# Kernel tuning notes

Measured on AMD Instinct MI355X. Metric: run time of the kernel, lower is better.

## Reference

```python
import jax, jax.numpy as jnp
import numpy as np

B, S, E, H = 2, 2048, 1024, 16
D = E // H  # head dim = 64
NEG_INF = -1e30


def alibi_slopes(n_head):
    # standard ALiBi slopes: 2^(-8*i/n_head), i = 1..n_head
    return jnp.asarray([2.0 ** (-8.0 * (i + 1) / n_head) for i in range(n_head)], dtype=jnp.float32)


def setup_inputs() -> dict:
    key = jax.random.key(0)
    ks = jax.random.split(key, 5)
    scale = 0.02
    return {
        "x": jax.random.normal(ks[0], (B, S, E), dtype=jnp.float32),
        "W_kqv": jax.random.normal(ks[1], (E, 3 * E), dtype=jnp.float32) * scale,
        "b_kqv": jnp.zeros((3 * E,), dtype=jnp.float32),
        "W_proj": jax.random.normal(ks[2], (E, E), dtype=jnp.float32) * scale,
        "b_proj": jnp.zeros((E,), dtype=jnp.float32),
        "slopes": alibi_slopes(H),
    }


def reference(x, W_kqv, b_kqv, W_proj, b_proj, slopes):
    b, s, e = x.shape
    kqv = x @ W_kqv + b_kqv                       # [b, s, 3e]
    k, q, v = jnp.split(kqv, 3, axis=-1)          # split order: k, q, v
    k = k.reshape(b, s, H, D)
    q = q.reshape(b, s, H, D)
    v = v.reshape(b, s, H, D)
    attn = jnp.einsum("bqhd,bkhd->bhqk", q, k) * (1.0 / jnp.sqrt(jnp.float32(D)))
    # ALiBi bias: slope_h * (j - i) for j <= i, -inf above diagonal (causal)
    i = jnp.arange(s)[:, None]
    j = jnp.arange(s)[None, :]
    rel = (j - i).astype(jnp.float32)             # [s, s]
    bias = slopes[:, None, None] * jnp.tril(rel)  # [h, s, s]
    bias = jnp.where(j > i, NEG_INF, bias)
    attn = jax.nn.softmax(attn + bias[None], axis=-1)
    # dropout is identity in eval mode
    y = jnp.einsum("bhqk,bkhd->bqhd", attn, v).reshape(b, s, e)
    return y @ W_proj + b_proj
```

## Files before the change

### kernel.cpp

```cpp
#include <hip/hip_runtime.h>

typedef unsigned short u16;
typedef float f32x4 __attribute__((ext_vector_type(4)));
typedef __bf16 bfx8 __attribute__((ext_vector_type(8)));
typedef __bf16 bfx4 __attribute__((ext_vector_type(4)));
typedef u16 u16x8 __attribute__((ext_vector_type(8)));
typedef u16 u16x4 __attribute__((ext_vector_type(4)));

#define B_ 2
#define S_ 2048
#define E_ 1024
#define H_ 16
#define D_ 64

__device__ __forceinline__ u16 f2bf(float f) {
  unsigned u = __float_as_uint(f);
  u = u + 0x7FFFu + ((u >> 16) & 1u);
  return (u16)(u >> 16);
}

__device__ __forceinline__ int swz128(int o) { return o ^ ((o >> 3) & 0x70); }

__device__ __forceinline__ void gload16(const void* g, void* l) {
  __builtin_amdgcn_global_load_lds((const __attribute__((address_space(1))) void*)g,
                                   (__attribute__((address_space(3))) void*)l, 16, 0, 0);
}

__global__ __launch_bounds__(256) void prep(const float* __restrict__ x,
                                            const float* __restrict__ Wk,
                                            const float* __restrict__ Wp, u16* __restrict__ xb,
                                            u16* __restrict__ wkt, u16* __restrict__ wpt) {
  __shared__ float tile[64][65];
  const int id = blockIdx.x, tid = threadIdx.x;
  if (id < 2048) {
    const float4* in4 = reinterpret_cast<const float4*>(x);
    u16x4* out4 = reinterpret_cast<u16x4*>(xb);
    int i = id * 256 + tid;
#pragma unroll
    for (int p = 0; p < 2; ++p, i += 524288) {
      const float4 v = in4[i];
      u16x4 o = {f2bf(v.x), f2bf(v.y), f2bf(v.z), f2bf(v.w)};
      out4[i] = o;
    }
    return;
  }
  const float* in;
  u16* out;
  int R, C, bx, by;
  if (id < 2816) {
    const int t = id - 2048;
    in = Wk; out = wkt; R = 1024; C = 3072; bx = t % 48; by = t / 48;
  } else {
    const int t = id - 2816;
    in = Wp; out = wpt; R = 1024; C = 1024; bx = t & 15; by = t >> 4;
  }
  const int ct = bx * 64, rt = by * 64;
#pragma unroll
  for (int p = 0; p < 4; ++p) {
    int f = p * 256 + tid;
    int row = f >> 4, c4 = (f & 15) << 2;
    const float4 v = *reinterpret_cast<const float4*>(in + (size_t)(rt + row) * C + ct + c4);
    tile[row][c4 + 0] = v.x; tile[row][c4 + 1] = v.y;
    tile[row][c4 + 2] = v.z; tile[row][c4 + 3] = v.w;
  }
  __syncthreads();
#pragma unroll
  for (int p = 0; p < 4; ++p) {
    int g = p * 256 + tid;
    int orow = g >> 4, k4 = (g & 15) << 2;
    u16x4 o = {f2bf(tile[k4 + 0][orow]), f2bf(tile[k4 + 1][orow]),
               f2bf(tile[k4 + 2][orow]), f2bf(tile[k4 + 3][orow])};
    *reinterpret_cast<u16x4*>(out + (size_t)(ct + orow) * R + rt + k4) = o;
  }
}

__global__ __launch_bounds__(256) void gemm_kqv(const u16* __restrict__ A,
                                                const u16* __restrict__ Bt,
                                                const float* __restrict__ bias, int M, int N, int K,
                                                u16* __restrict__ outK, u16* __restrict__ outQ,
                                                u16* __restrict__ outVt) {
  __shared__ __align__(16) u16 sA[128 * 64];
  __shared__ __align__(16) u16 sB[128 * 64];
  const int tid = threadIdx.x, lane = tid & 63;
  const int wave = tid >> 6, wr = wave >> 1, wc = wave & 1;
  int lin = blockIdx.y * gridDim.x + blockIdx.x;
  const int nwg = gridDim.x * gridDim.y;
  if ((nwg & 7) == 0) {
    const int cpx = nwg >> 3;
    lin = (lin & 7) * cpx + (lin >> 3);
  }
  const int bm = (lin / gridDim.x) * 128, bn = (lin % gridDim.x) * 128;
  const int r8 = lane >> 3, c16 = (lane & 7) ^ r8;
  f32x4 acc[4][4] = {};
  for (int k0 = 0; k0 < K; k0 += 64) {
#pragma unroll
    for (int i = 0; i < 4; ++i) {
      const int c = wave * 4 + i;
      const int row = c * 8 + r8;
      gload16(A + (size_t)(bm + row) * K + k0 + c16 * 8, (char*)sA + c * 1024);
      gload16(Bt + (size_t)(bn + row) * K + k0 + c16 * 8, (char*)sB + c * 1024);
    }
    __syncthreads();
#pragma unroll
    for (int kc = 0; kc < 2; ++kc) {
      bfx8 af[4], bf[4];
#pragma unroll
      for (int mf = 0; mf < 4; ++mf) {
        int o = swz128(((wr * 64 + mf * 16 + (lane & 15)) << 7) + kc * 64 + ((lane >> 4) << 4));
        af[mf] = *reinterpret_cast<const bfx8*>(reinterpret_cast<const char*>(sA) + o);
      }
#pragma unroll
      for (int nf = 0; nf < 4; ++nf) {
        int o = swz128(((wc * 64 + nf * 16 + (lane & 15)) << 7) + kc * 64 + ((lane >> 4) << 4));
        bf[nf] = *reinterpret_cast<const bfx8*>(reinterpret_cast<const char*>(sB) + o);
      }
#pragma unroll
      for (int mf = 0; mf < 4; ++mf)
#pragma unroll
        for (int nf = 0; nf < 4; ++nf)
          acc[mf][nf] = __builtin_amdgcn_mfma_f32_16x16x32_bf16(af[mf], bf[nf], acc[mf][nf], 0, 0, 0);
    }
    __syncthreads();
  }
#pragma unroll
  for (int mf = 0; mf < 4; ++mf)
#pragma unroll
    for (int nf = 0; nf < 4; ++nf)
#pragma unroll
      for (int r = 0; r < 4; ++r) {
        const int row = bm + wr * 64 + mf * 16 + ((lane >> 4) << 2) + r;
        const int col = bn + wc * 64 + nf * 16 + (lane & 15);
        const float v = acc[mf][nf][r] + bias[col];
        const int chunk = col >> 10, w = col & 1023, h = w >> 6, dd = w & 63;
        const int b = row >> 11, s = row & 2047;
        const int bh = b * H_ + h;
        if (chunk == 0)
          outK[((size_t)bh * S_ + s) * D_ + dd] = f2bf(v);
        else if (chunk == 1)
          outQ[((size_t)bh * S_ + s) * D_ + dd] = f2bf(v);
        else
          outVt[((size_t)bh * D_ + dd) * S_ + s] = f2bf(v);
      }
}

__global__ __launch_bounds__(512) void gemm_proj(const u16* __restrict__ A,
                                                 const u16* __restrict__ Bt,
                                                 const float* __restrict__ bias, int M, int N,
                                                 int K, float* __restrict__ outF) {
  __shared__ __align__(16) u16 sA[128 * 64];
  __shared__ __align__(16) u16 sB[128 * 64];
  const int tid = threadIdx.x, lane = tid & 63;
  const int wave = tid >> 6, wr = wave >> 2, wc = wave & 3;
  int lin = blockIdx.y * gridDim.x + blockIdx.x;
  const int nwg = gridDim.x * gridDim.y;
  if ((nwg & 7) == 0) {
    const int cpx = nwg >> 3;
    lin = (lin & 7) * cpx + (lin >> 3);
  }
  const int bm = (lin / gridDim.x) * 128, bn = (lin % gridDim.x) * 128;
  const int r8 = lane >> 3, c16 = (lane & 7) ^ r8;
  f32x4 acc[4][2] = {};
  for (int k0 = 0; k0 < K; k0 += 64) {
#pragma unroll
    for (int i = 0; i < 2; ++i) {
      const int c = wave * 2 + i;
      const int row = c * 8 + r8;
      gload16(A + (size_t)(bm + row) * K + k0 + c16 * 8, (char*)sA + c * 1024);
      gload16(Bt + (size_t)(bn + row) * K + k0 + c16 * 8, (char*)sB + c * 1024);
    }
    __syncthreads();
#pragma unroll
    for (int kc = 0; kc < 2; ++kc) {
      bfx8 af[4], bf[2];
#pragma unroll
      for (int mf = 0; mf < 4; ++mf) {
        int o = swz128(((wr * 64 + mf * 16 + (lane & 15)) << 7) + kc * 64 + ((lane >> 4) << 4));
        af[mf] = *reinterpret_cast<const bfx8*>(reinterpret_cast<const char*>(sA) + o);
      }
#pragma unroll
      for (int nf = 0; nf < 2; ++nf) {
        int o = swz128(((wc * 32 + nf * 16 + (lane & 15)) << 7) + kc * 64 + ((lane >> 4) << 4));
        bf[nf] = *reinterpret_cast<const bfx8*>(reinterpret_cast<const char*>(sB) + o);
      }
#pragma unroll
      for (int mf = 0; mf < 4; ++mf)
#pragma unroll
        for (int nf = 0; nf < 2; ++nf)
          acc[mf][nf] = __builtin_amdgcn_mfma_f32_16x16x32_bf16(af[mf], bf[nf], acc[mf][nf], 0, 0, 0);
    }
    __syncthreads();
  }
#pragma unroll
  for (int mf = 0; mf < 4; ++mf)
#pragma unroll
    for (int nf = 0; nf < 2; ++nf)
#pragma unroll
      for (int r = 0; r < 4; ++r) {
        const int row = bm + wr * 64 + mf * 16 + ((lane >> 4) << 2) + r;
        const int col = bn + wc * 32 + nf * 16 + (lane & 15);
        outF[(size_t)row * N + col] = acc[mf][nf][r] + bias[col];
      }
}

__global__ __launch_bounds__(256, 4) void attn_alibi(const u16* __restrict__ Q,
                                                     const u16* __restrict__ Kb,
                                                     const u16* __restrict__ Vt,
                                                     const float* __restrict__ slopes,
                                                     u16* __restrict__ Y) {
  __shared__ __align__(16) u16 sK[2][4096];
  __shared__ __align__(16) u16 sV[2][4096];
  __shared__ __align__(16) __bf16 sP[4][16 * 64];
  const int id = blockIdx.x;
  const int xcd = id & 7, w = id >> 3;
  const int bh = xcd * 4 + (w >> 5);
  const int r5 = w & 31;
  const int qi = ((w >> 5) & 1) ? r5 : 31 - r5;
  const int b = bh >> 4, h = bh & 15;
  const int tid = threadIdx.x, lane = tid & 63, wave = tid >> 6;
  const int q = lane & 15, g = lane >> 4;
  const int q0 = qi * 64;
  const int w0 = q0 + wave * 16;
  const float L2E = 1.44269504089f;
  const float SCALE = 0.125f * L2E;
  const float sl2 = slopes[h] * L2E;
  const size_t headSD = (size_t)bh * (S_ * D_);
  const size_t headDS = (size_t)bh * (D_ * S_);
  const int nt = qi + 1;
  const int r8 = lane >> 3, c16 = (lane & 7) ^ r8;

  bfx8 qf[2];
  {
    const u16* qp = Q + headSD + (size_t)(w0 + q) * D_ + g * 8;
    qf[0] = *reinterpret_cast<const bfx8*>(qp);
    qf[1] = *reinterpret_cast<const bfx8*>(qp + 32);
  }
  bfx8 onesf;
#pragma unroll
  for (int j = 0; j < 8; ++j) onesf[j] = (__bf16)1.0f;
  f32x4 base[4];
#pragma unroll
  for (int nf = 0; nf < 4; ++nf)
#pragma unroll
    for (int r = 0; r < 4; ++r) base[nf][r] = sl2 * (float)(nf * 16 + 4 * g + r);
  const int ir0 = wave * 16 + q;

  float m = 0.f;
  f32x4 oT[4] = {};
  f32x4 oX = {};

  auto stage = [&](int t, int buf) {
#pragma unroll
    for (int i = 0; i < 2; ++i) {
      const int c = wave * 2 + i;
      const int row = c * 8 + r8;
      gload16(Kb + headSD + (size_t)t * 4096 + row * 64 + c16 * 8, (char*)sK[buf] + c * 1024);
      gload16(Vt + headDS + (size_t)row * S_ + t * 64 + c16 * 8, (char*)sV[buf] + c * 1024);
    }
  };

  stage(0, 0);
  __syncthreads();
  int cur = 0;
  for (int t = 0; t < nt; ++t) {
    if (t + 1 < nt) stage(t + 1, cur ^ 1);
    const char* sKc = reinterpret_cast<const char*>(sK[cur]);
    const char* sVc = reinterpret_cast<const char*>(sV[cur]);
    f32x4 tt[4] = {};
    __builtin_amdgcn_s_setprio(1);
#pragma unroll
    for (int kc = 0; kc < 2; ++kc)
#pragma unroll
      for (int nf = 0; nf < 4; ++nf) {
        const bfx8 kf =
            *reinterpret_cast<const bfx8*>(sKc + swz128(((nf * 16 + q) << 7) + kc * 64 + (g << 4)));
        tt[nf] = __builtin_amdgcn_mfma_f32_16x16x32_bf16(kf, qf[kc], tt[nf], 0, 0, 0);
      }
    __builtin_amdgcn_s_setprio(0);
    const float tb = sl2 * (float)(t * 64);
    if (t != nt - 1) {
      float rmax = -3.0e38f;
#pragma unroll
      for (int nf = 0; nf < 4; ++nf)
#pragma unroll
        for (int r = 0; r < 4; ++r) rmax = fmaxf(rmax, tt[nf][r]);
      rmax = fmaxf(rmax, __shfl_xor(rmax, 16));
      rmax = fmaxf(rmax, __shfl_xor(rmax, 32));
      const float bound = fmaf(rmax, SCALE, tb + sl2 * 63.f);
      if (!__all(bound <= m + 12.0f)) {
        const float mnew = fmaxf(m, bound);
        const float corr = __builtin_amdgcn_exp2f(m - mnew);
        m = mnew;
#pragma unroll
        for (int nf = 0; nf < 4; ++nf) oT[nf] *= corr;
        oX *= corr;
      }
      const float tbm = tb - m;
#pragma unroll
      for (int nf = 0; nf < 4; ++nf) {
        const f32x4 bb = base[nf] + tbm;
#pragma unroll
        for (int r = 0; r < 4; ++r)
          tt[nf][r] = __builtin_amdgcn_exp2f(fmaf(tt[nf][r], SCALE, bb[r]));
      }
    } else {
      float rmax = -3.0e38f;
#pragma unroll
      for (int nf = 0; nf < 4; ++nf)
#pragma unroll
        for (int r = 0; r < 4; ++r) {
          float sv = fmaf(tt[nf][r], SCALE, base[nf][r] + tb);
          if (nf * 16 + 4 * g + r > ir0) sv = -3.0e38f;
          tt[nf][r] = sv;
          rmax = fmaxf(rmax, sv);
        }
      rmax = fmaxf(rmax, __shfl_xor(rmax, 16));
      rmax = fmaxf(rmax, __shfl_xor(rmax, 32));
      if (!__all(rmax <= m + 12.0f)) {
        const float mnew = fmaxf(m, rmax);
        const float corr = __builtin_amdgcn_exp2f(m - mnew);
        m = mnew;
#pragma unroll
        for (int nf = 0; nf < 4; ++nf) oT[nf] *= corr;
        oX *= corr;
      }
#pragma unroll
      for (int nf = 0; nf < 4; ++nf)
#pragma unroll
        for (int r = 0; r < 4; ++r) tt[nf][r] = __builtin_amdgcn_exp2f(tt[nf][r] - m);
    }
    char* pw = reinterpret_cast<char*>(sP[wave]);
#pragma unroll
    for (int nf = 0; nf < 4; ++nf) {
      bfx4 w = {(__bf16)tt[nf][0], (__bf16)tt[nf][1], (__bf16)tt[nf][2], (__bf16)tt[nf][3]};
      *reinterpret_cast<bfx4*>(pw + swz128((q << 7) + nf * 32 + g * 8)) = w;
    }
    bfx8 pa[2];
#pragma unroll
    for (int kc = 0; kc < 2; ++kc)
      pa[kc] = *reinterpret_cast<const bfx8*>(pw + swz128((q << 7) + kc * 64 + (g << 4)));
    __builtin_amdgcn_s_setprio(1);
#pragma unroll
    for (int kc = 0; kc < 2; ++kc) {
#pragma unroll
      for (int nf = 0; nf < 4; ++nf) {
        const bfx8 vf =
            *reinterpret_cast<const bfx8*>(sVc + swz128(((nf * 16 + q) << 7) + kc * 64 + (g << 4)));
        oT[nf] = __builtin_amdgcn_mfma_f32_16x16x32_bf16(vf, pa[kc], oT[nf], 0, 0, 0);
      }
      oX = __builtin_amdgcn_mfma_f32_16x16x32_bf16(onesf, pa[kc], oX, 0, 0, 0);
    }
    __builtin_amdgcn_s_setprio(0);
    __syncthreads();
    cur ^= 1;
  }
  const float rl = 1.0f / oX[0];
  const int row = w0 + q;
#pragma unroll
  for (int nf = 0; nf < 4; ++nf) {
    bfx4 w = {(__bf16)(oT[nf][0] * rl), (__bf16)(oT[nf][1] * rl), (__bf16)(oT[nf][2] * rl),
              (__bf16)(oT[nf][3] * rl)};
    const int col = h * 64 + nf * 16 + g * 4;
    *reinterpret_cast<bfx4*>(reinterpret_cast<char*>(Y) + (((size_t)b * S_ + row) * E_ + col) * 2) =
        w;
  }
}

extern "C" void kernel_launch(void* const* d_in, const int* in_sizes, int n_in, void* d_out,
                              int out_size, void* d_ws, size_t ws_size, hipStream_t stream) {
  (void)in_sizes; (void)n_in; (void)out_size; (void)ws_size;
  const float* x = (const float*)d_in[0];
  const float* Wkqv = (const float*)d_in[1];
  const float* bkqv = (const float*)d_in[2];
  const float* Wproj = (const float*)d_in[3];
  const float* bproj = (const float*)d_in[4];
  const float* slopes = (const float*)d_in[5];
  float* out = (float*)d_out;

  const size_t MBE = (size_t)4096 * 1024;
  u16* xb = (u16*)d_ws;
  u16* wkqvt = xb + MBE;
  u16* wprojt = wkqvt + (size_t)3072 * 1024;
  u16* kbuf = wprojt + (size_t)1024 * 1024;
  u16* qbuf = kbuf + MBE;
  u16* vtbuf = qbuf + MBE;
  u16* ybuf = vtbuf + MBE;

  prep<<<dim3(3072), dim3(256), 0, stream>>>(x, Wkqv, Wproj, xb, wkqvt, wprojt);
  gemm_kqv<<<dim3(24, 32), dim3(256), 0, stream>>>(xb, wkqvt, bkqv, 4096, 3072, 1024, kbuf, qbuf,
                                                   vtbuf);
  attn_alibi<<<dim3(1024), dim3(256), 0, stream>>>(qbuf, kbuf, vtbuf, slopes, ybuf);
  gemm_proj<<<dim3(8, 32), dim3(512), 0, stream>>>(ybuf, wprojt, bproj, 4096, 1024, 1024, out);
}
```

Baseline: 118.3 us.

## Split long causal attention rows into KV chunks with a separate merge kernel

```diff
diff --git a/kernel.cpp b/kernel.cpp
--- a/kernel.cpp
+++ b/kernel.cpp
@@ -25,6 +25,23 @@
   __builtin_amdgcn_global_load_lds((const __attribute__((address_space(1))) void*)g,
                                    (__attribute__((address_space(3))) void*)l, 16, 0, 0);
 }
+
+__device__ const signed char TQI[60] = {31, 31, 30, 30, 29, 29, 28, 28, 27, 27, 26, 26, 25, 25, 24,
+                                        24, 23, 23, 22, 21, 20, 19, 18, 17, 16, 15, 14, 13, 12, 11,
+                                        22, 10, 21, 9,  20, 8,  31, 19, 7,  30, 18, 6,  29, 17, 5,
+                                        28, 16, 4,  27, 15, 3,  26, 14, 2,  25, 13, 1,  24, 12, 0};
+__device__ const signed char TT0[60] = {0,  12, 0,  12, 0,  12, 0,  12, 0,  12, 0,  12, 0,  12, 0,
+                                        12, 0,  12, 0,  0,  0,  0,  0,  0,  0,  0,  0,  0,  0,  0,
+                                        12, 0,  12, 0,  12, 0,  24, 12, 0,  24, 12, 0,  24, 12, 0,
+                                        24, 12, 0,  24, 12, 0,  24, 12, 0,  24, 12, 0,  24, 12, 0};
+__device__ const signed char TT1[60] = {12, 24, 12, 24, 12, 24, 12, 24, 12, 24, 12, 24, 12, 24, 12,
+                                        24, 12, 24, 12, 12, 12, 12, 12, 12, 12, 12, 12, 12, 12, 12,
+                                        23, 11, 22, 10, 21, 9,  32, 20, 8,  31, 19, 7,  30, 18, 6,
+                                        29, 17, 5,  28, 16, 4,  27, 15, 3,  26, 14, 2,  25, 13, 1};
+__device__ const signed char TSL[60] = {45, 46, 42, 43, 39, 40, 36, 37, 33, 34, 30, 31, 27, 28, 24,
+                                        25, 22, 23, 20, 18, 16, 14, 12, 10, 8,  6,  4,  2,  0,  -1,
+                                        21, -1, 19, -1, 17, -1, 47, 15, -1, 44, 13, -1, 41, 11, -1,
+                                        38, 9,  -1, 35, 7,  -1, 32, 5,  -1, 29, 3,  -1, 26, 1,  -1};
 
 __global__ __launch_bounds__(256) void prep(const float* __restrict__ x,
                                             const float* __restrict__ Wk,
@@ -206,15 +223,16 @@
                                                      const u16* __restrict__ Kb,
                                                      const u16* __restrict__ Vt,
                                                      const float* __restrict__ slopes,
-                                                     u16* __restrict__ Y) {
+                                                     u16* __restrict__ Y, u16* __restrict__ pO,
+                                                     float* __restrict__ pML) {
   __shared__ __align__(16) u16 sK[2][4096];
   __shared__ __align__(16) u16 sV[2][4096];
   __shared__ __align__(16) __bf16 sP[4][16 * 64];
   const int id = blockIdx.x;
-  const int xcd = id & 7, w = id >> 3;
-  const int bh = xcd * 4 + (w >> 5);
-  const int r5 = w & 31;
-  const int qi = ((w >> 5) & 1) ? r5 : 31 - r5;
+  const int xcd = id & 7, j = id >> 3;
+  const int bh = xcd * 4 + (j & 3);
+  const int c = j >> 2;
+  const int qi = TQI[c], t0 = TT0[c], t1 = TT1[c], slot = TSL[c];
   const int b = bh >> 4, h = bh & 15;
   const int tid = threadIdx.x, lane = tid & 63, wave = tid >> 6;
   const int q = lane & 15, g = lane >> 4;
@@ -225,7 +243,6 @@
   const float sl2 = slopes[h] * L2E;
   const size_t headSD = (size_t)bh * (S_ * D_);
   const size_t headDS = (size_t)bh * (D_ * S_);
-  const int nt = qi + 1;
   const int r8 = lane >> 3, c16 = (lane & 7) ^ r8;
 
   bfx8 qf[2];
@@ -236,7 +253,7 @@
   }
   bfx8 onesf;
 #pragma unroll
-  for (int j = 0; j < 8; ++j) onesf[j] = (__bf16)1.0f;
+  for (int jj = 0; jj < 8; ++jj) onesf[jj] = (__bf16)1.0f;
   f32x4 base[4];
 #pragma unroll
   for (int nf = 0; nf < 4; ++nf)
@@ -251,18 +268,18 @@
   auto stage = [&](int t, int buf) {
 #pragma unroll
     for (int i = 0; i < 2; ++i) {
-      const int c = wave * 2 + i;
-      const int row = c * 8 + r8;
-      gload16(Kb + headSD + (size_t)t * 4096 + row * 64 + c16 * 8, (char*)sK[buf] + c * 1024);
-      gload16(Vt + headDS + (size_t)row * S_ + t * 64 + c16 * 8, (char*)sV[buf] + c * 1024);
+      const int cc = wave * 2 + i;
+      const int row = cc * 8 + r8;
+      gload16(Kb + headSD + (size_t)t * 4096 + row * 64 + c16 * 8, (char*)sK[buf] + cc * 1024);
+      gload16(Vt + headDS + (size_t)row * S_ + t * 64 + c16 * 8, (char*)sV[buf] + cc * 1024);
     }
   };
 
-  stage(0, 0);
+  stage(t0, 0);
   __syncthreads();
   int cur = 0;
-  for (int t = 0; t < nt; ++t) {
-    if (t + 1 < nt) stage(t + 1, cur ^ 1);
+  for (int t = t0; t < t1; ++t) {
+    if (t + 1 < t1) stage(t + 1, cur ^ 1);
     const char* sKc = reinterpret_cast<const char*>(sK[cur]);
     const char* sVc = reinterpret_cast<const char*>(sV[cur]);
     f32x4 tt[4] = {};
@@ -277,7 +294,7 @@
       }
     __builtin_amdgcn_s_setprio(0);
     const float tb = sl2 * (float)(t * 64);
-    if (t != nt - 1) {
+    if (t != qi) {
       float rmax = -3.0e38f;
 #pragma unroll
       for (int nf = 0; nf < 4; ++nf)
@@ -353,16 +370,85 @@
     __syncthreads();
     cur ^= 1;
   }
-  const float rl = 1.0f / oX[0];
-  const int row = w0 + q;
-#pragma unroll
-  for (int nf = 0; nf < 4; ++nf) {
-    bfx4 w = {(__bf16)(oT[nf][0] * rl), (__bf16)(oT[nf][1] * rl), (__bf16)(oT[nf][2] * rl),
-              (__bf16)(oT[nf][3] * rl)};
-    const int col = h * 64 + nf * 16 + g * 4;
-    *reinterpret_cast<bfx4*>(reinterpret_cast<char*>(Y) + (((size_t)b * S_ + row) * E_ + col) * 2) =
-        w;
-  }
+  if (slot < 0) {
+    const float rl = 1.0f / oX[0];
+    const int row = w0 + q;
+#pragma unroll
+    for (int nf = 0; nf < 4; ++nf) {
+      bfx4 w = {(__bf16)(oT[nf][0] * rl), (__bf16)(oT[nf][1] * rl), (__bf16)(oT[nf][2] * rl),
+                (__bf16)(oT[nf][3] * rl)};
+      const int col = h * 64 + nf * 16 + g * 4;
+      *reinterpret_cast<bfx4*>(reinterpret_cast<char*>(Y) +
+                               (((size_t)b * S_ + row) * E_ + col) * 2) = w;
+    }
+  } else {
+    const int sg = bh * 48 + slot;
+    u16* po = pO + (size_t)sg * 4096 + (size_t)(wave * 16 + q) * 64;
+#pragma unroll
+    for (int nf = 0; nf < 4; ++nf) {
+      bfx4 w = {(__bf16)oT[nf][0], (__bf16)oT[nf][1], (__bf16)oT[nf][2], (__bf16)oT[nf][3]};
+      *reinterpret_cast<bfx4*>(po + nf * 16 + g * 4) = w;
+    }
+    if (g == 0) {
+      float2 ml = make_float2(m, oX[0]);
+      reinterpret_cast<float2*>(pML)[sg * 64 + wave * 16 + q] = ml;
+    }
+  }
+}
+
+__global__ __launch_bounds__(256) void merge_attn(const u16* __restrict__ pO,
+                                                  const float* __restrict__ pML,
+                                                  u16* __restrict__ Y) {
+  const int mb = blockIdx.x;
+  const int bh = mb / 20, qq = mb % 20, qi = 12 + qq;
+  const int nch = (qi < 24) ? 2 : 3;
+  const int sb = (qi < 24) ? (qi - 12) * 2 : 24 + (qi - 24) * 3;
+  const int b = bh >> 4, h = bh & 15;
+  const int tid = threadIdx.x;
+  const int r = tid >> 2, dq = (tid & 3) * 16;
+  const float2* ml2 = reinterpret_cast<const float2*>(pML);
+  float mm[3], ll[3];
+  float M = -3.0e38f;
+#pragma unroll
+  for (int c = 0; c < 3; ++c) {
+    if (c < nch) {
+      const float2 v = ml2[(bh * 48 + sb + c) * 64 + r];
+      mm[c] = v.x;
+      ll[c] = v.y;
+      M = fmaxf(M, v.x);
+    } else {
+      mm[c] = -3.0e38f;
+      ll[c] = 0.f;
+    }
+  }
+  float L = 0.f, acc[16];
+#pragma unroll
+  for (int i = 0; i < 16; ++i) acc[i] = 0.f;
+#pragma unroll
+  for (int c = 0; c < 3; ++c) {
+    if (c < nch) {
+      const float w = __builtin_amdgcn_exp2f(mm[c] - M);
+      L += w * ll[c];
+      const u16* src = pO + (size_t)(bh * 48 + sb + c) * 4096 + r * 64 + dq;
+      const u16x8 a = *reinterpret_cast<const u16x8*>(src);
+      const u16x8 bb = *reinterpret_cast<const u16x8*>(src + 8);
+#pragma unroll
+      for (int i = 0; i < 8; ++i) {
+        acc[i] += w * __uint_as_float(((unsigned)a[i]) << 16);
+        acc[8 + i] += w * __uint_as_float(((unsigned)bb[i]) << 16);
+      }
+    }
+  }
+  const float rl = 1.0f / L;
+  u16x8 o0, o1;
+#pragma unroll
+  for (int i = 0; i < 8; ++i) {
+    o0[i] = f2bf(acc[i] * rl);
+    o1[i] = f2bf(acc[8 + i] * rl);
+  }
+  u16* dst = Y + ((size_t)b * S_ + qi * 64 + r) * E_ + h * 64 + dq;
+  *reinterpret_cast<u16x8*>(dst) = o0;
+  *reinterpret_cast<u16x8*>(dst + 8) = o1;
 }
 
 extern "C" void kernel_launch(void* const* d_in, const int* in_sizes, int n_in, void* d_out,
@@ -384,10 +470,13 @@
   u16* qbuf = kbuf + MBE;
   u16* vtbuf = qbuf + MBE;
   u16* ybuf = vtbuf + MBE;
+  u16* pO = xb;
+  float* pML = (float*)(xb + (size_t)1536 * 4096);
 
   prep<<<dim3(3072), dim3(256), 0, stream>>>(x, Wkqv, Wproj, xb, wkqvt, wprojt);
   gemm_kqv<<<dim3(24, 32), dim3(256), 0, stream>>>(xb, wkqvt, bkqv, 4096, 3072, 1024, kbuf, qbuf,
                                                    vtbuf);
-  attn_alibi<<<dim3(1024), dim3(256), 0, stream>>>(qbuf, kbuf, vtbuf, slopes, ybuf);
+  attn_alibi<<<dim3(1920), dim3(256), 0, stream>>>(qbuf, kbuf, vtbuf, slopes, ybuf, pO, pML);
+  merge_attn<<<dim3(640), dim3(256), 0, stream>>>(pO, pML, ybuf);
   gemm_proj<<<dim3(8, 32), dim3(512), 0, stream>>>(ybuf, wprojt, bproj, 4096, 1024, 1024, out);
 }
```

New measurement: 115.0 us. 2.7% less time.
